# Kernel tuning notes

Measured on AMD Instinct MI355X. Metric: run time of the kernel, lower is better.

The kernel has to match this reference:

```python
import jax, jax.numpy as jnp
import numpy as np

B, S, R, H = 16, 2048, 196, 768


def setup_inputs() -> dict:
    key = jax.random.key(0)
    ks = jax.random.split(key, 7)
    sc = 1.0 / np.sqrt(H)
    return {
        "text_features": jax.random.normal(ks[0], (B, S, H), jnp.float32),
        "img_features": jax.random.normal(ks[1], (B, R, H), jnp.float32),
        "W_text": jax.random.normal(ks[2], (H, H), jnp.float32) * sc,
        "b_text": jax.random.normal(ks[3], (H,), jnp.float32) * sc,
        "W_img": jax.random.normal(ks[4], (H, H), jnp.float32) * sc,
        "w_att": jax.random.normal(ks[5], (2 * H,), jnp.float32) * sc,
        "b_att": jax.random.normal(ks[6], (1,), jnp.float32) * sc,
    }


def reference(text_features, img_features, W_text, b_text, W_img, w_att, b_att):
    # Original: repeat text over regions, repeat img over seq, project, concat,
    # tanh, score via att_linear, softmax over regions, weighted sum of img.
    # tanh(concat(t, i)) = concat(tanh(t), tanh(i)), and the concat linear
    # splits into two dot products, so we avoid materializing (B,S,R,2H).
    H_ = text_features.shape[-1]
    t = jnp.tanh(jnp.einsum('bsh,oh->bso', text_features, W_text) + b_text)  # (B,S,H)
    i = jnp.tanh(jnp.einsum('brh,oh->bro', img_features, W_img))             # (B,R,H)
    w1, w2 = w_att[:H_], w_att[H_:]
    # score[b,s,r] = t[b,s]@w1 + i[b,r]@w2 + b_att
    scores = (t @ w1)[:, :, None] + (i @ w2)[:, None, :] + b_att[0]          # (B,S,R)
    att = jax.nn.softmax(scores, axis=-1)
    # weighted sum over regions of the ORIGINAL img features
    return jnp.einsum('bsr,brh->bsh', att, img_features)                      # (B,S,H)
```

## Files before the change

### kernel.cpp

```cpp
#include <hip/hip_runtime.h>
#include <math.h>

#define Bb   16
#define Ss   2048
#define Rr   196
#define Hh   768
#define Mtot (Bb * Rr)
#define NT   (Hh / 64)
#define LDA  72

typedef __attribute__((ext_vector_type(8))) short short8;
typedef __attribute__((ext_vector_type(4))) short short4v;
typedef __attribute__((ext_vector_type(4))) float f32x4;

__device__ inline short f2bf(float f) {
    unsigned u = __builtin_bit_cast(unsigned, f);
    u += 0x7fff + ((u >> 16) & 1);
    return (short)(u >> 16);
}

__global__ __launch_bounds__(256) void k0_cvt(
    const f32x4* __restrict__ a, short4v* __restrict__ da, int na4,
    const f32x4* __restrict__ b, short4v* __restrict__ db)
{
    int gid = blockIdx.x * 256 + threadIdx.x;
    const f32x4* s;
    short4v* d;
    int i;
    if (gid < na4) { s = a; d = da; i = gid; }
    else           { s = b; d = db; i = gid - na4; }
    f32x4 x = s[i];
    short4v o;
    o.x = f2bf(x.x); o.y = f2bf(x.y); o.z = f2bf(x.z); o.w = f2bf(x.w);
    d[i] = o;
}

template <bool FROM_F32>
__global__ __launch_bounds__(256) void k1_mfma(
    const void* __restrict__ Ap, const void* __restrict__ Bp,
    const float* __restrict__ w_att, float* __restrict__ part)
{
    const int m0   = blockIdx.x * 64;
    const int n0   = blockIdx.y * 64;
    const int t    = threadIdx.x;
    const int lane = t & 63;
    const int wv   = t >> 6;
    const int wm   = (wv & 1) * 32;
    const int wn   = (wv >> 1) * 32;
    const int col  = lane & 15;
    const int quad = lane >> 4;

    __shared__ short As[64 * LDA];
    __shared__ short Bs[64 * LDA];
    __shared__ float red[64][2];

    f32x4 acc[2][2] = {};

    const int sm = t >> 2;
    const int sq = t & 3;

    for (int k0 = 0; k0 < Hh; k0 += 64) {
        short8 areg[2], breg[2];
        if (FROM_F32) {
            const float* A = (const float*)Ap;
            const float* B = (const float*)Bp;
#pragma unroll
            for (int j = 0; j < 2; ++j) {
                float4 lo = *(const float4*)&A[(size_t)(m0 + sm) * Hh + k0 + sq * 16 + j * 8];
                float4 hi = *(const float4*)&A[(size_t)(m0 + sm) * Hh + k0 + sq * 16 + j * 8 + 4];
                areg[j][0] = f2bf(lo.x); areg[j][1] = f2bf(lo.y);
                areg[j][2] = f2bf(lo.z); areg[j][3] = f2bf(lo.w);
                areg[j][4] = f2bf(hi.x); areg[j][5] = f2bf(hi.y);
                areg[j][6] = f2bf(hi.z); areg[j][7] = f2bf(hi.w);
                lo = *(const float4*)&B[(size_t)(n0 + sm) * Hh + k0 + sq * 16 + j * 8];
                hi = *(const float4*)&B[(size_t)(n0 + sm) * Hh + k0 + sq * 16 + j * 8 + 4];
                breg[j][0] = f2bf(lo.x); breg[j][1] = f2bf(lo.y);
                breg[j][2] = f2bf(lo.z); breg[j][3] = f2bf(lo.w);
                breg[j][4] = f2bf(hi.x); breg[j][5] = f2bf(hi.y);
                breg[j][6] = f2bf(hi.z); breg[j][7] = f2bf(hi.w);
            }
        } else {
            const short* A = (const short*)Ap;
            const short* B = (const short*)Bp;
#pragma unroll
            for (int j = 0; j < 2; ++j) {
                areg[j] = *(const short8*)&A[(size_t)(m0 + sm) * Hh + k0 + sq * 16 + j * 8];
                breg[j] = *(const short8*)&B[(size_t)(n0 + sm) * Hh + k0 + sq * 16 + j * 8];
            }
        }
        __syncthreads();
#pragma unroll
        for (int j = 0; j < 2; ++j) {
            *(short8*)&As[sm * LDA + sq * 16 + j * 8] = areg[j];
            *(short8*)&Bs[sm * LDA + sq * 16 + j * 8] = breg[j];
        }
        __syncthreads();
#pragma unroll
        for (int kk = 0; kk < 64; kk += 32) {
            short8 a0 = *(const short8*)&As[(wm +      col) * LDA + kk + quad * 8];
            short8 a1 = *(const short8*)&As[(wm + 16 + col) * LDA + kk + quad * 8];
            short8 b0 = *(const short8*)&Bs[(wn +      col) * LDA + kk + quad * 8];
            short8 b1 = *(const short8*)&Bs[(wn + 16 + col) * LDA + kk + quad * 8];
            acc[0][0] = __builtin_amdgcn_mfma_f32_16x16x32_bf16(a0, b0, acc[0][0], 0, 0, 0);
            acc[0][1] = __builtin_amdgcn_mfma_f32_16x16x32_bf16(a0, b1, acc[0][1], 0, 0, 0);
            acc[1][0] = __builtin_amdgcn_mfma_f32_16x16x32_bf16(a1, b0, acc[1][0], 0, 0, 0);
            acc[1][1] = __builtin_amdgcn_mfma_f32_16x16x32_bf16(a1, b1, acc[1][1], 0, 0, 0);
        }
    }

    const float* w2 = w_att + Hh;
    float w2v0 = w2[n0 + wn + col];
    float w2v1 = w2[n0 + wn + 16 + col];

#pragma unroll
    for (int mi = 0; mi < 2; ++mi) {
#pragma unroll
        for (int r = 0; r < 4; ++r) {
            float s = tanhf(acc[mi][0][r]) * w2v0 + tanhf(acc[mi][1][r]) * w2v1;
            s += __shfl_xor(s, 1, 64);
            s += __shfl_xor(s, 2, 64);
            s += __shfl_xor(s, 4, 64);
            s += __shfl_xor(s, 8, 64);
            if (col == 0)
                red[wm + mi * 16 + quad * 4 + r][wn >> 5] = s;
        }
    }
    __syncthreads();
    if (t < 64)
        part[blockIdx.y * Mtot + m0 + t] = red[t][0] + red[t][1];
}

__global__ __launch_bounds__(256) void k2_softmax_v(
    const float* __restrict__ part,
    const float* __restrict__ img,
    float* __restrict__ v)
{
    const int b = blockIdx.x;
    const int t = threadIdx.x;

    __shared__ float p[Rr];
    __shared__ float redbuf[256];
    __shared__ float a2[4][65];

    float myv = -INFINITY;
    if (t < Rr) {
        float s = 0.f;
#pragma unroll
        for (int nt = 0; nt < NT; ++nt) s += part[nt * Mtot + b * Rr + t];
        p[t] = s;
        myv = s;
    }
    redbuf[t] = myv;
    __syncthreads();
    for (int off = 128; off > 0; off >>= 1) {
        if (t < off) redbuf[t] = fmaxf(redbuf[t], redbuf[t + off]);
        __syncthreads();
    }
    const float mx = redbuf[0];
    __syncthreads();

    float e = 0.f;
    if (t < Rr) e = expf(p[t] - mx);
    redbuf[t] = e;
    __syncthreads();
    for (int off = 128; off > 0; off >>= 1) {
        if (t < off) redbuf[t] += redbuf[t + off];
        __syncthreads();
    }
    const float inv = 1.f / redbuf[0];
    __syncthreads();
    if (t < Rr) p[t] = e * inv;
    __syncthreads();

    const int h  = blockIdx.y * 64 + (t & 63);
    const int rg = t >> 6;
    const float* imgb = img + (size_t)b * Rr * Hh + h;
    float s = 0.f;
#pragma unroll 7
    for (int r = rg * 49; r < rg * 49 + 49; ++r)
        s = fmaf(p[r], imgb[(size_t)r * Hh], s);
    a2[rg][t & 63] = s;
    __syncthreads();
    if (t < 64)
        v[b * Hh + blockIdx.y * 64 + t] = a2[0][t] + a2[1][t] + a2[2][t] + a2[3][t];
}

__global__ __launch_bounds__(256) void k3_bcast(
    const f32x4* __restrict__ v4,
    f32x4* __restrict__ out)
{
    const int gid   = blockIdx.x * 256 + threadIdx.x;
    const int per_b = Ss * (Hh / 4);
    const int b     = gid / per_b;
    const int h4    = gid % (Hh / 4);
    f32x4 val = v4[b * (Hh / 4) + h4];
    __builtin_nontemporal_store(val, &out[gid]);
}

extern "C" void kernel_launch(void* const* d_in, const int* in_sizes, int n_in,
                              void* d_out, int out_size, void* d_ws, size_t ws_size,
                              hipStream_t stream)
{
    const float* img   = (const float*)d_in[1];
    const float* W_img = (const float*)d_in[4];
    const float* w_att = (const float*)d_in[5];

    float* part = (float*)d_ws;
    float* v    = part + NT * Mtot;
    size_t off  = ((size_t)(NT * Mtot + Bb * Hh) * 4 + 15) & ~(size_t)15;
    short* imgbf = (short*)((char*)d_ws + off);
    short* Wbf   = imgbf + (size_t)Mtot * Hh;
    const size_t need = off + ((size_t)Mtot * Hh + (size_t)Hh * Hh) * 2;

    float* out = (float*)d_out;
    const bool usebf = (ws_size >= need);

    if (usebf) {
        const int na4 = (Mtot * Hh) / 4;
        const int nb4 = (Hh * Hh) / 4;
        k0_cvt<<<(na4 + nb4) / 256, 256, 0, stream>>>(
            (const f32x4*)img, (short4v*)imgbf, na4,
            (const f32x4*)W_img, (short4v*)Wbf);
        k1_mfma<false><<<dim3(Mtot / 64, NT), 256, 0, stream>>>(imgbf, Wbf, w_att, part);
    } else {
        k1_mfma<true><<<dim3(Mtot / 64, NT), 256, 0, stream>>>(img, W_img, w_att, part);
    }

    k2_softmax_v<<<dim3(Bb, NT), 256, 0, stream>>>(part, img, v);

    const int total4 = Bb * Ss * (Hh / 4);
    k3_bcast<<<total4 / 256, 256, 0, stream>>>((const f32x4*)v, (f32x4*)out);
}
```

Measured before the change: 194.0 us.

## Double the GEMM K-tile and prefetch the next tile into registers during MFMA

The projection GEMM now uses a K tile of 128 instead of 64, which halves the number of barrier pairs. It also loads the next tile's global data into registers while the current shared-memory tile feeds the MFMAs, so global load latency can overlap compute. In exchange it raises register and LDS use per block, which may reduce occupancy. The kernel time is likely dominated by the large broadcast write, so the gain is limited to the GEMM part.

```diff
diff --git a/kernel.cpp b/kernel.cpp
--- a/kernel.cpp
+++ b/kernel.cpp
@@ -7,7 +7,8 @@
 #define Hh   768
 #define Mtot (Bb * Rr)
 #define NT   (Hh / 64)
-#define LDA  72
+#define BK   128
+#define LDA  136
 
 typedef __attribute__((ext_vector_type(8))) short short8;
 typedef __attribute__((ext_vector_type(4))) short short4v;
@@ -59,44 +60,78 @@
     const int sm = t >> 2;
     const int sq = t & 3;
 
-    for (int k0 = 0; k0 < Hh; k0 += 64) {
-        short8 areg[2], breg[2];
-        if (FROM_F32) {
-            const float* A = (const float*)Ap;
-            const float* B = (const float*)Bp;
-#pragma unroll
-            for (int j = 0; j < 2; ++j) {
-                float4 lo = *(const float4*)&A[(size_t)(m0 + sm) * Hh + k0 + sq * 16 + j * 8];
-                float4 hi = *(const float4*)&A[(size_t)(m0 + sm) * Hh + k0 + sq * 16 + j * 8 + 4];
-                areg[j][0] = f2bf(lo.x); areg[j][1] = f2bf(lo.y);
-                areg[j][2] = f2bf(lo.z); areg[j][3] = f2bf(lo.w);
-                areg[j][4] = f2bf(hi.x); areg[j][5] = f2bf(hi.y);
-                areg[j][6] = f2bf(hi.z); areg[j][7] = f2bf(hi.w);
-                lo = *(const float4*)&B[(size_t)(n0 + sm) * Hh + k0 + sq * 16 + j * 8];
-                hi = *(const float4*)&B[(size_t)(n0 + sm) * Hh + k0 + sq * 16 + j * 8 + 4];
-                breg[j][0] = f2bf(lo.x); breg[j][1] = f2bf(lo.y);
-                breg[j][2] = f2bf(lo.z); breg[j][3] = f2bf(lo.w);
-                breg[j][4] = f2bf(hi.x); breg[j][5] = f2bf(hi.y);
-                breg[j][6] = f2bf(hi.z); breg[j][7] = f2bf(hi.w);
+    short8 areg[4], breg[4];
+
+    if (FROM_F32) {
+        const float* A = (const float*)Ap;
+        const float* B = (const float*)Bp;
+#pragma unroll
+        for (int j = 0; j < 4; ++j) {
+            float4 lo = *(const float4*)&A[(size_t)(m0 + sm) * Hh + sq * 32 + j * 8];
+            float4 hi = *(const float4*)&A[(size_t)(m0 + sm) * Hh + sq * 32 + j * 8 + 4];
+            areg[j][0] = f2bf(lo.x); areg[j][1] = f2bf(lo.y);
+            areg[j][2] = f2bf(lo.z); areg[j][3] = f2bf(lo.w);
+            areg[j][4] = f2bf(hi.x); areg[j][5] = f2bf(hi.y);
+            areg[j][6] = f2bf(hi.z); areg[j][7] = f2bf(hi.w);
+            lo = *(const float4*)&B[(size_t)(n0 + sm) * Hh + sq * 32 + j * 8];
+            hi = *(const float4*)&B[(size_t)(n0 + sm) * Hh + sq * 32 + j * 8 + 4];
+            breg[j][0] = f2bf(lo.x); breg[j][1] = f2bf(lo.y);
+            breg[j][2] = f2bf(lo.z); breg[j][3] = f2bf(lo.w);
+            breg[j][4] = f2bf(hi.x); breg[j][5] = f2bf(hi.y);
+            breg[j][6] = f2bf(hi.z); breg[j][7] = f2bf(hi.w);
+        }
+    } else {
+        const short* A = (const short*)Ap;
+        const short* B = (const short*)Bp;
+#pragma unroll
+        for (int j = 0; j < 4; ++j) {
+            areg[j] = *(const short8*)&A[(size_t)(m0 + sm) * Hh + sq * 32 + j * 8];
+            breg[j] = *(const short8*)&B[(size_t)(n0 + sm) * Hh + sq * 32 + j * 8];
+        }
+    }
+
+    for (int k0 = 0; k0 < Hh; k0 += BK) {
+        __syncthreads();
+#pragma unroll
+        for (int j = 0; j < 4; ++j) {
+            *(short8*)&As[sm * LDA + sq * 32 + j * 8] = areg[j];
+            *(short8*)&Bs[sm * LDA + sq * 32 + j * 8] = breg[j];
+        }
+        __syncthreads();
+
+        if (k0 + BK < Hh) {
+            const int kn = k0 + BK;
+            if (FROM_F32) {
+                const float* A = (const float*)Ap;
+                const float* B = (const float*)Bp;
+#pragma unroll
+                for (int j = 0; j < 4; ++j) {
+                    float4 lo = *(const float4*)&A[(size_t)(m0 + sm) * Hh + kn + sq * 32 + j * 8];
+                    float4 hi = *(const float4*)&A[(size_t)(m0 + sm) * Hh + kn + sq * 32 + j * 8 + 4];
+                    areg[j][0] = f2bf(lo.x); areg[j][1] = f2bf(lo.y);
+                    areg[j][2] = f2bf(lo.z); areg[j][3] = f2bf(lo.w);
+                    areg[j][4] = f2bf(hi.x); areg[j][5] = f2bf(hi.y);
+                    areg[j][6] = f2bf(hi.z); areg[j][7] = f2bf(hi.w);
+                    lo = *(const float4*)&B[(size_t)(n0 + sm) * Hh + kn + sq * 32 + j * 8];
+                    hi = *(const float4*)&B[(size_t)(n0 + sm) * Hh + kn + sq * 32 + j * 8 + 4];
+                    breg[j][0] = f2bf(lo.x); breg[j][1] = f2bf(lo.y);
+                    breg[j][2] = f2bf(lo.z); breg[j][3] = f2bf(lo.w);
+                    breg[j][4] = f2bf(hi.x); breg[j][5] = f2bf(hi.y);
+                    breg[j][6] = f2bf(hi.z); breg[j][7] = f2bf(hi.w);
+                }
+            } else {
+                const short* A = (const short*)Ap;
+                const short* B = (const short*)Bp;
+#pragma unroll
+                for (int j = 0; j < 4; ++j) {
+                    areg[j] = *(const short8*)&A[(size_t)(m0 + sm) * Hh + kn + sq * 32 + j * 8];
+                    breg[j] = *(const short8*)&B[(size_t)(n0 + sm) * Hh + kn + sq * 32 + j * 8];
+                }
             }
-        } else {
-            const short* A = (const short*)Ap;
-            const short* B = (const short*)Bp;
-#pragma unroll
-            for (int j = 0; j < 2; ++j) {
-                areg[j] = *(const short8*)&A[(size_t)(m0 + sm) * Hh + k0 + sq * 16 + j * 8];
-                breg[j] = *(const short8*)&B[(size_t)(n0 + sm) * Hh + k0 + sq * 16 + j * 8];
-            }
-        }
-        __syncthreads();
-#pragma unroll
-        for (int j = 0; j < 2; ++j) {
-            *(short8*)&As[sm * LDA + sq * 16 + j * 8] = areg[j];
-            *(short8*)&Bs[sm * LDA + sq * 16 + j * 8] = breg[j];
-        }
-        __syncthreads();
-#pragma unroll
-        for (int kk = 0; kk < 64; kk += 32) {
+        }
+
+#pragma unroll
+        for (int kk = 0; kk < BK; kk += 32) {
             short8 a0 = *(const short8*)&As[(wm +      col) * LDA + kk + quad * 8];
             short8 a1 = *(const short8*)&As[(wm + 16 + col) * LDA + kk + quad * 8];
             short8 b0 = *(const short8*)&Bs[(wn +      col) * LDA + kk + quad * 8];
```

Result: slower. 198.6 us (+2.4%).
